# Performance work log

Measured on AMD Instinct MI355X. Metric: run time of the kernel, lower is better.

The kernel has to match this reference:

```python
import jax, jax.numpy as jnp
import numpy as np

B = 32768   # num_agents
D = 512     # obs_dim
H = 1024    # hidden_dim
O = 8       # num_options
A = 16      # num_actions
SCALE = 0.02


def setup_inputs() -> dict:
    key = jax.random.key(0)
    ks = jax.random.split(key, 12)
    rn = lambda k, shape: (jax.random.normal(k, shape, jnp.float32) * SCALE)
    obs = jax.random.normal(ks[0], (B, D), jnp.float32)
    dones = jax.random.bernoulli(ks[1], 0.05, (B,))
    executing_option = jax.random.randint(ks[2], (B,), 0, O)
    return {
        "obs": obs,
        "dones": dones,
        "executing_option": executing_option,
        # meta policy params
        "Wm1": rn(ks[3], (D, H)), "bm1": jnp.zeros((H,), jnp.float32),
        "Wm_pi": rn(ks[4], (H, O)), "Wm_v": rn(ks[5], (H, 1)),
        # termination net params (per-option sigmoid heads)
        "Wt1": rn(ks[6], (D, H)), "Wt2": rn(ks[7], (H, O)),
        # per-option sub-policy params (stacked over options)
        "W1": rn(ks[8], (O, D, H)), "b1": jnp.zeros((O, H), jnp.float32),
        "Wpi": rn(ks[9], (O, H, A)), "Wv": rn(ks[10], (O, H, 1)),
    }


def reference(obs, dones, executing_option,
              Wm1, bm1, Wm_pi, Wm_v, Wt1, Wt2, W1, b1, Wpi, Wv):
    # ---- meta policy: option logits + value + log_prob of chosen option ----
    hm = jax.nn.relu(obs @ Wm1 + bm1)                       # [B, H]
    meta_logits = hm @ Wm_pi                                # [B, O]
    meta_logp_all = jax.nn.log_softmax(meta_logits, axis=-1)
    meta_actions = jnp.argmax(meta_logits, axis=-1)         # [B]
    meta_log_probs = jnp.take_along_axis(meta_logp_all, meta_actions[:, None], 1)[:, 0]
    meta_values = (hm @ Wm_v)[:, 0]                         # [B]

    # ---- termination: per-option sigmoid head, gathered at executing option ----
    ht = jax.nn.relu(obs @ Wt1)                             # [B, H]
    term_all = jax.nn.sigmoid(ht @ Wt2)                     # [B, O]
    termination_probs = jnp.take_along_axis(term_all, executing_option[:, None], 1)[:, 0]
    option_terminates = dones | (termination_probs > 0.5)
    new_option = jnp.where(option_terminates, meta_actions, executing_option)  # [B]

    # ---- per-option sub-policy dispatch (dense compute, masked select) ----
    actions = jnp.zeros((obs.shape[0],), meta_actions.dtype)
    values = jnp.full((obs.shape[0],), jnp.nan, obs.dtype)
    log_probs = jnp.full((obs.shape[0],), jnp.nan, obs.dtype)
    for o in range(O):  # small fixed option set (structurally distinct experts)
        mask = new_option == o                              # [B]
        h = jax.nn.relu(obs @ W1[o] + b1[o])                # [B, H]
        logits = h @ Wpi[o]                                 # [B, A]
        logp_all = jax.nn.log_softmax(logits, axis=-1)
        act = jnp.argmax(logits, axis=-1)                   # [B]
        lp = jnp.take_along_axis(logp_all, act[:, None], 1)[:, 0]
        val = (h @ Wv[o])[:, 0]                             # [B]
        actions = jnp.where(mask, act, actions)
        values = jnp.where(mask, val, values)
        log_probs = jnp.where(mask, lp, log_probs)

    return (actions, values, log_probs,
            meta_actions, meta_values, meta_log_probs, termination_probs)
```

## Files before the change

### kernel.cpp

```cpp
#include <hip/hip_runtime.h>


constexpr int Bn = 32768;
constexpr int Dk = 512;
constexpr int Hn = 1024;

typedef __attribute__((ext_vector_type(8))) short short8v;
typedef __attribute__((ext_vector_type(4))) float f32x4;

__device__ __forceinline__ unsigned short f2bf(float x) {
    unsigned u = __float_as_uint(x);
    u += 0x7FFFu + ((u >> 16) & 1u);
    return (unsigned short)(u >> 16);
}
__device__ __forceinline__ float bf2f(unsigned short h) {
    return __uint_as_float(((unsigned)h) << 16);
}

constexpr size_t WS_COUNTS  = 0;
constexpr size_t WS_DFLAG   = 32;
constexpr size_t WS_BUCKETS = 64;
constexpr size_t WS_LOGITS  = 1u << 20;
constexpr size_t LOG_SZ     = (size_t)Bn * 20 * 4;
constexpr size_t WS_HID     = 16u << 20;
constexpr size_t WS_HEAD    = 40u << 20;
constexpr size_t WS_NEED    = WS_HEAD + (size_t)10 * 2 * 32 * 1024 * 2;

__global__ void k_detect(const unsigned int* __restrict__ w, int* __restrict__ flag)
{
    unsigned int acc = 0;
    for (int i = threadIdx.x; i < 8192; i += blockDim.x) acc |= w[i];
    if (acc & 0xFFFFFF00u) atomicOr(flag, 1);
}

__global__ __launch_bounds__(256)
void k_split_hid(const float* __restrict__ Wm1, const float* __restrict__ Wt1,
                 const float* __restrict__ W1, unsigned short* __restrict__ dst)
{
    const int bid = blockIdx.x;
    const int m  = bid >> 7;
    const int t  = bid & 127;
    const int k0 = (t >> 4) << 6;
    const int n0 = (t & 15) << 6;
    const float* src = (m == 0) ? Wm1 : (m == 1) ? Wt1 : (W1 + (size_t)(m - 2) * Dk * Hn);

    __shared__ unsigned short sT[2][64][72];
    const int tid = threadIdx.x;
    const int kk = tid >> 2;
    const int nc = (tid & 3) << 4;
    const float* p = src + (size_t)(k0 + kk) * Hn + n0 + nc;
#pragma unroll
    for (int i = 0; i < 4; ++i) {
        const float4 v = *(const float4*)(p + i * 4);
        float xs[4] = {v.x, v.y, v.z, v.w};
#pragma unroll
        for (int e = 0; e < 4; ++e) {
            const unsigned short h = f2bf(xs[e]);
            const unsigned short l = f2bf(xs[e] - bf2f(h));
            sT[0][nc + i * 4 + e][kk] = h;
            sT[1][nc + i * 4 + e][kk] = l;
        }
    }
    __syncthreads();
    if (tid < 128) {
        const int pl = tid >> 6, n = tid & 63;
        unsigned short* dp = dst + ((size_t)(m * 2 + pl) * 1024 + n0 + n) * 512 + k0;
        const unsigned short* sp = &sT[pl][n][0];
#pragma unroll
        for (int i = 0; i < 8; ++i)
            *(short8v*)(dp + i * 8) = *(const short8v*)(sp + i * 8);
    }
}

__global__ __launch_bounds__(256)
void k_split_head(const float* __restrict__ Wm_pi, const float* __restrict__ Wm_v,
                  const float* __restrict__ Wt2, const float* __restrict__ Wpi,
                  const float* __restrict__ Wv, unsigned short* __restrict__ dst)
{
    const int set = blockIdx.x >> 5, c = blockIdx.x & 31;
    const int tid = threadIdx.x;
    unsigned short* d0 = dst + ((size_t)(set * 2 + 0) * 32 + c) * 1024;
    unsigned short* d1 = dst + ((size_t)(set * 2 + 1) * 32 + c) * 1024;
#pragma unroll
    for (int i = 0; i < 4; ++i) {
        const int k = tid + i * 256;
        float x = 0.f;
        if (set == 0)      { if (c < 8) x = Wm_pi[k * 8 + c]; else if (c == 8) x = Wm_v[k]; }
        else if (set == 1) { if (c < 8) x = Wt2[k * 8 + c]; }
        else { const int o = set - 2;
               if (c < 16) x = Wpi[((size_t)o * 1024 + k) * 16 + c];
               else if (c == 16) x = Wv[o * 1024 + k]; }
        const unsigned short h = f2bf(x);
        d0[k] = h;
        d1[k] = f2bf(x - bf2f(h));
    }
}

template<int MODE, int CT>
__global__ __launch_bounds__(256, 2)
void k_gemm(const float* __restrict__ obs,
            const unsigned short* __restrict__ hidPl,
            const unsigned short* __restrict__ headPl,
            const float* __restrict__ bm1,
            const float* __restrict__ b1,
            float* __restrict__ L,
            const int* __restrict__ counts,
            const unsigned short* __restrict__ buckets)
{
    __shared__ __align__(16) unsigned char s_raw[65536];
    __shared__ float s_bias[128];
    __shared__ int   s_idx[128];

    const int tid = threadIdx.x;
    const int bid = blockIdx.x;

    int mat, set, ch, nrows = 128;
    const float* bias = nullptr;

    if constexpr (MODE == 2) {
        const int o = bid >> 11, rem = bid & 2047;
        const int x = rem & 7;  ch = (rem >> 3) & 7;
        const int rt = x + ((rem >> 6) << 3);
        const int n = counts[o], start = rt << 7;
        if (start >= n) return;
        nrows = min(128, n - start);
        if (tid < 128) s_idx[tid] = (int)buckets[(o << 15) + start + min(tid, nrows - 1)];
        mat = 2 + o; set = 2 + o; bias = b1 + (size_t)o * Hn;
    } else {
        const int x = bid & 7;  ch = (bid >> 3) & 7;
        const int rt = x + ((bid >> 6) << 3);
        if (tid < 128) s_idx[tid] = (rt << 7) + tid;
        mat = MODE; set = MODE; bias = (MODE == 0) ? bm1 : nullptr;
    }
    const int hc = ch << 7;
    if (tid < 128) s_bias[tid] = (MODE == 1) ? 0.f : bias[hc + tid];
    __syncthreads();

    const int l = tid & 63, w = tid >> 6;
    const int r15 = l & 15, q = l >> 4;
    const int R0 = (w >> 1) * 64, C0 = (w & 1) * 64;

    const int arow = tid >> 1, ahalf = tid & 1;
    const int bpl = tid >> 7, bn = tid & 127;
    const size_t arowg = (size_t)s_idx[arow] * Dk;
    const unsigned short* bptr = hidPl + ((size_t)(mat * 2 + bpl) * 1024 + (hc + bn)) * 512;

    f32x4 acc[4][4];
#pragma unroll
    for (int i = 0; i < 4; ++i)
#pragma unroll
        for (int j = 0; j < 4; ++j) acc[i][j] = (f32x4){0.f, 0.f, 0.f, 0.f};

    float4  av[4];
    short8v bv[4];

    auto stage_load = [&](int kt) {
        const float* p = obs + arowg + kt * 32 + ahalf * 16;
        av[0] = *(const float4*)(p);      av[1] = *(const float4*)(p + 4);
        av[2] = *(const float4*)(p + 8);  av[3] = *(const float4*)(p + 12);
        const unsigned short* bp = bptr + kt * 32;
#pragma unroll
        for (int j = 0; j < 4; ++j) bv[j] = *(const short8v*)(bp + j * 8);
    };

    auto stage_write = [&](int buf) {
        float xs[16] = {av[0].x, av[0].y, av[0].z, av[0].w,  av[1].x, av[1].y, av[1].z, av[1].w,
                        av[2].x, av[2].y, av[2].z, av[2].w,  av[3].x, av[3].y, av[3].z, av[3].w};
        short8v H0, H1, Lo0, Lo1;
#pragma unroll
        for (int e = 0; e < 8; ++e) {
            unsigned short h = f2bf(xs[e]);
            H0[e] = (short)h;  Lo0[e] = (short)f2bf(xs[e] - bf2f(h));
            h = f2bf(xs[8 + e]);
            H1[e] = (short)h;  Lo1[e] = (short)f2bf(xs[8 + e] - bf2f(h));
        }
        const int sw  = (arow >> 1) & 3;
        const int ra  = arow * 64;
        unsigned char* a0 = s_raw + (buf * 2 + 0) * 8192 + ra;
        unsigned char* a1 = s_raw + (buf * 2 + 1) * 8192 + ra;
        const int q0 = ((2 * ahalf) ^ sw) << 4, q1 = ((2 * ahalf + 1) ^ sw) << 4;
        *(short8v*)(a0 + q0) = H0;  *(short8v*)(a0 + q1) = H1;
        *(short8v*)(a1 + q0) = Lo0; *(short8v*)(a1 + q1) = Lo1;

        const int swb = (bn >> 1) & 3;
        unsigned char* bb = s_raw + 32768 + (buf * 2 + bpl) * 8192 + bn * 64;
#pragma unroll
        for (int j = 0; j < 4; ++j)
            *(short8v*)(bb + ((j ^ swb) << 4)) = bv[j];
    };

    auto mfma_step = [&](int buf) {
        short8v a[2][4], b[2][4];
#pragma unroll
        for (int rf = 0; rf < 4; ++rf) {
            const int row = R0 + rf * 16 + r15;
            const int off = row * 64 + ((q ^ ((row >> 1) & 3)) << 4);
            a[0][rf] = *(const short8v*)(s_raw + (buf * 2 + 0) * 8192 + off);
            a[1][rf] = *(const short8v*)(s_raw + (buf * 2 + 1) * 8192 + off);
        }
#pragma unroll
        for (int cf = 0; cf < 4; ++cf) {
            const int n = C0 + cf * 16 + r15;
            const int off = n * 64 + ((q ^ ((n >> 1) & 3)) << 4);
            b[0][cf] = *(const short8v*)(s_raw + 32768 + (buf * 2 + 0) * 8192 + off);
            b[1][cf] = *(const short8v*)(s_raw + 32768 + (buf * 2 + 1) * 8192 + off);
        }
#pragma unroll
        for (int t = 0; t < 4; ++t) {
            const int pa = 1 - (t >> 1), pb = 1 - (t & 1);
#pragma unroll
            for (int rf = 0; rf < 4; ++rf)
#pragma unroll
                for (int cf = 0; cf < 4; ++cf)
                    acc[rf][cf] = __builtin_amdgcn_mfma_f32_16x16x32_bf16(
                        a[pa][rf], b[pb][cf], acc[rf][cf], 0, 0, 0);
        }
    };

    stage_load(0);
    stage_write(0);
    __syncthreads();
#pragma unroll 1
    for (int kt = 0; kt < 16; ++kt) {
        const int cb = kt & 1;
        if (kt < 15) stage_load(kt + 1);
        mfma_step(cb);
        if (kt < 15) stage_write(cb ^ 1);
        __syncthreads();
    }

    {
        const int pl = tid >> 7, idx = tid & 127, c = idx >> 2, kq = idx & 3;
        const unsigned short* hp = headPl + ((size_t)(set * 2 + pl) * 32 + c) * 1024 + hc + kq * 32;
        short8v h0 = *(const short8v*)(hp);      short8v h1 = *(const short8v*)(hp + 8);
        short8v h2 = *(const short8v*)(hp + 16); short8v h3 = *(const short8v*)(hp + 24);
        unsigned char* d = s_raw + 33792 + pl * 8704 + c * 272 + kq * 64;
        ((short8v*)d)[0] = h0; ((short8v*)d)[1] = h1; ((short8v*)d)[2] = h2; ((short8v*)d)[3] = h3;
    }

    float* sh = (float*)s_raw;
#pragma unroll 1
    for (int half = 0; half < 2; ++half) {
        if ((w >> 1) == half) {
#pragma unroll
            for (int rf = 0; rf < 4; ++rf)
#pragma unroll
                for (int cf = 0; cf < 4; ++cf) {
                    const int c = C0 + cf * 16 + r15;
                    const float bs = s_bias[c];
#pragma unroll
                    for (int reg = 0; reg < 4; ++reg) {
                        const int r = rf * 16 + q * 4 + reg;
                        sh[r * 132 + c] = fmaxf(acc[rf][cf][reg] + bs, 0.f);
                    }
                }
        }
        __syncthreads();

        f32x4 hacc[2];
        hacc[0] = (f32x4){0.f, 0.f, 0.f, 0.f};
        hacc[1] = (f32x4){0.f, 0.f, 0.f, 0.f};
#pragma unroll
        for (int ks = 0; ks < 4; ++ks) {
            const float* shp = sh + (w * 16 + r15) * 132 + ks * 32 + q * 8;
            const float4 f0 = *(const float4*)(shp);
            const float4 f1 = *(const float4*)(shp + 4);
            const float xs[8] = {f0.x, f0.y, f0.z, f0.w, f1.x, f1.y, f1.z, f1.w};
            short8v ah, al;
#pragma unroll
            for (int j = 0; j < 8; ++j) {
                const unsigned short h = f2bf(xs[j]);
                ah[j] = (short)h;
                al[j] = (short)f2bf(xs[j] - bf2f(h));
            }
#pragma unroll
            for (int cf = 0; cf < 2; ++cf) {
                const unsigned char* hb = s_raw + 33792 + (cf * 16 + r15) * 272 + ks * 64 + q * 16;
                const short8v b0 = *(const short8v*)(hb);
                const short8v b1 = *(const short8v*)(hb + 8704);
                hacc[cf] = __builtin_amdgcn_mfma_f32_16x16x32_bf16(al, b1, hacc[cf], 0, 0, 0);
                hacc[cf] = __builtin_amdgcn_mfma_f32_16x16x32_bf16(al, b0, hacc[cf], 0, 0, 0);
                hacc[cf] = __builtin_amdgcn_mfma_f32_16x16x32_bf16(ah, b1, hacc[cf], 0, 0, 0);
                hacc[cf] = __builtin_amdgcn_mfma_f32_16x16x32_bf16(ah, b0, hacc[cf], 0, 0, 0);
            }
        }
#pragma unroll
        for (int cf = 0; cf < 2; ++cf) {
            const int c = cf * 16 + r15;
            if (c < CT) {
#pragma unroll
                for (int reg = 0; reg < 4; ++reg) {
                    const int rl = half * 64 + w * 16 + q * 4 + reg;
                    if (rl < nrows)
                        atomicAdd(&L[(size_t)s_idx[rl] * 20 + c], hacc[cf][reg]);
                }
            }
        }
        __syncthreads();
    }
}

__global__ __launch_bounds__(256)
void k_epi_meta(const float* __restrict__ L, float* __restrict__ out)
{
    const int g = blockIdx.x * 256 + threadIdx.x;
    const float* lr = L + (size_t)g * 20;
    float m = lr[0]; int am = 0;
#pragma unroll
    for (int j = 1; j < 8; ++j) { const float x = lr[j]; if (x > m) { m = x; am = j; } }
    float s = 0.f;
#pragma unroll
    for (int j = 0; j < 8; ++j) s += expf(lr[j] - m);
    out[3 * Bn + g] = (float)am;
    out[4 * Bn + g] = lr[8];
    out[5 * Bn + g] = -logf(s);
}

__global__ __launch_bounds__(256)
void k_epi_term(const float* __restrict__ L, float* __restrict__ out,
                const int* __restrict__ execopt, const void* __restrict__ dones,
                const int* __restrict__ dflag, int* __restrict__ counts,
                unsigned short* __restrict__ buckets)
{
    const int g = blockIdx.x * 256 + threadIdx.x;
    const int eo = execopt[g];
    const float logit = L[(size_t)g * 20 + eo];
    const float p = 1.f / (1.f + expf(-logit));
    out[6 * Bn + g] = p;
    bool dn;
    if (*dflag) dn = ((const unsigned char*)dones)[g] != 0;
    else        dn = ((const int*)dones)[g] != 0;
    const int ma = (int)out[3 * Bn + g];
    const int no = (dn || (p > 0.5f)) ? ma : eo;
    const int pos = atomicAdd(&counts[no], 1);
    buckets[(no << 15) + pos] = (unsigned short)g;
}

__global__ __launch_bounds__(256)
void k_epi_sub(const float* __restrict__ L, float* __restrict__ out)
{
    const int g = blockIdx.x * 256 + threadIdx.x;
    const float* lr = L + (size_t)g * 20;
    float m = lr[0]; int am = 0;
#pragma unroll
    for (int j = 1; j < 16; ++j) { const float x = lr[j]; if (x > m) { m = x; am = j; } }
    float s = 0.f;
#pragma unroll
    for (int j = 0; j < 16; ++j) s += expf(lr[j] - m);
    out[0 * Bn + g] = (float)am;
    out[1 * Bn + g] = lr[16];
    out[2 * Bn + g] = -logf(s);
}

constexpr int FB_ROWS = 64;
constexpr int FB_HC   = 128;
constexpr int FB_KT   = 16;
constexpr int FB_NT   = 256;

template<int CA, int CB, bool HASBIAS, int MODE>
__global__ __launch_bounds__(FB_NT, 2)
void k_fused_fb(const float* __restrict__ obs, const float* __restrict__ WhB,
                const float* __restrict__ biasB, const float* __restrict__ WAB,
                const float* __restrict__ WBB, float* __restrict__ out,
                int* __restrict__ counts, unsigned short* __restrict__ buckets,
                const void* __restrict__ dones, const int* __restrict__ dflag,
                const int* __restrict__ execopt)
{
    constexpr int CT  = CA + CB;
    constexpr int CPT = (CT + 3) / 4;

    __shared__ float s_obsT[FB_KT][FB_ROWS + 4];
    __shared__ float s_W[FB_KT][FB_HC + 4];
    __shared__ float s_h[FB_ROWS][FB_HC + 4];
    __shared__ float s_WhT[17][FB_HC + 4];
    __shared__ float s_logits[FB_ROWS][20];
    __shared__ float s_bias[FB_HC];
    __shared__ int   s_idx[FB_ROWS];

    const int tid = threadIdx.x;
    int nrows = FB_ROWS;
    const float* Wh = WhB; const float* bias = biasB;
    const float* WA = WAB; const float* WB = WBB;

    if constexpr (MODE == 2) {
        const int o = blockIdx.x >> 9;
        const int t = blockIdx.x & 511;
        const int n = counts[o];
        const int start = t * FB_ROWS;
        if (start >= n) return;
        nrows = min(FB_ROWS, n - start);
        if (tid < FB_ROWS) s_idx[tid] = (int)buckets[o * Bn + start + min(tid, nrows - 1)];
        Wh = WhB + (size_t)o * Dk * Hn; bias = biasB + (size_t)o * Hn;
        WA = WAB + (size_t)o * Hn * 16; WB = WBB + (size_t)o * Hn;
    } else {
        if (tid < FB_ROWS) s_idx[tid] = blockIdx.x * FB_ROWS + tid;
    }
    __syncthreads();

    const int tc = tid & 15, tr = tid >> 4;
    const int hr = tid >> 2, hq = tid & 3;
    const int ld_row = tid >> 2, ld_kk = (tid & 3) * 4;

    float head_acc[CPT];
#pragma unroll
    for (int i = 0; i < CPT; ++i) head_acc[i] = 0.f;

    for (int hcc = 0; hcc < Hn; hcc += FB_HC) {
        for (int e = tid; e < CT * FB_HC; e += FB_NT) {
            const int c = e >> 7, j = e & (FB_HC - 1);
            float v;
            if (c < CA) v = WA[(size_t)(hcc + j) * CA + c];
            else        v = WB[(size_t)(hcc + j) * CB + (c - CA)];
            s_WhT[c][j] = v;
        }
        if constexpr (HASBIAS) { if (tid < FB_HC) s_bias[tid] = bias[hcc + tid]; }

        float acc[4][8];
#pragma unroll
        for (int i = 0; i < 4; ++i)
#pragma unroll
            for (int j = 0; j < 8; ++j) acc[i][j] = 0.f;

        for (int kt = 0; kt < Dk; kt += FB_KT) {
            __syncthreads();
            {
                const int gr = s_idx[ld_row];
                const float4 v = *reinterpret_cast<const float4*>(obs + (size_t)gr * Dk + kt + ld_kk);
                s_obsT[ld_kk + 0][ld_row] = v.x; s_obsT[ld_kk + 1][ld_row] = v.y;
                s_obsT[ld_kk + 2][ld_row] = v.z; s_obsT[ld_kk + 3][ld_row] = v.w;
            }
#pragma unroll
            for (int p = 0; p < 2; ++p) {
                const int Li = tid + p * FB_NT;
                const int k = Li >> 5, cg = (Li & 31) * 4;
                *reinterpret_cast<float4*>(&s_W[k][cg]) =
                    *reinterpret_cast<const float4*>(Wh + (size_t)(kt + k) * Hn + hcc + cg);
            }
            __syncthreads();
#pragma unroll
            for (int k = 0; k < FB_KT; ++k) {
                const float4 avv = *reinterpret_cast<const float4*>(&s_obsT[k][tr * 4]);
                const float4 b0 = *reinterpret_cast<const float4*>(&s_W[k][tc * 4]);
                const float4 b1 = *reinterpret_cast<const float4*>(&s_W[k][64 + tc * 4]);
                float a_[4] = {avv.x, avv.y, avv.z, avv.w};
                float b_[8] = {b0.x, b0.y, b0.z, b0.w, b1.x, b1.y, b1.z, b1.w};
#pragma unroll
                for (int i = 0; i < 4; ++i)
#pragma unroll
                    for (int j = 0; j < 8; ++j) acc[i][j] = fmaf(a_[i], b_[j], acc[i][j]);
            }
        }

#pragma unroll
        for (int i = 0; i < 4; ++i) {
            const int r = tr * 4 + i;
            float4 v0, v1;
            v0.x = acc[i][0]; v0.y = acc[i][1]; v0.z = acc[i][2]; v0.w = acc[i][3];
            v1.x = acc[i][4]; v1.y = acc[i][5]; v1.z = acc[i][6]; v1.w = acc[i][7];
            if constexpr (HASBIAS) {
                v0.x += s_bias[tc * 4 + 0]; v0.y += s_bias[tc * 4 + 1];
                v0.z += s_bias[tc * 4 + 2]; v0.w += s_bias[tc * 4 + 3];
                v1.x += s_bias[64 + tc * 4 + 0]; v1.y += s_bias[64 + tc * 4 + 1];
                v1.z += s_bias[64 + tc * 4 + 2]; v1.w += s_bias[64 + tc * 4 + 3];
            }
            v0.x = fmaxf(v0.x, 0.f); v0.y = fmaxf(v0.y, 0.f);
            v0.z = fmaxf(v0.z, 0.f); v0.w = fmaxf(v0.w, 0.f);
            v1.x = fmaxf(v1.x, 0.f); v1.y = fmaxf(v1.y, 0.f);
            v1.z = fmaxf(v1.z, 0.f); v1.w = fmaxf(v1.w, 0.f);
            *reinterpret_cast<float4*>(&s_h[r][tc * 4]) = v0;
            *reinterpret_cast<float4*>(&s_h[r][64 + tc * 4]) = v1;
        }
        __syncthreads();
        {
            const float* hrow = s_h[hr];
#pragma unroll
            for (int i = 0; i < CPT; ++i) {
                const int c = hq * CPT + i;
                if (c < CT) {
                    const float* wrow = s_WhT[c];
                    float a = head_acc[i];
#pragma unroll
                    for (int j = 0; j < FB_HC; j += 4) {
                        const float4 hv = *reinterpret_cast<const float4*>(&hrow[j]);
                        const float4 wv = *reinterpret_cast<const float4*>(&wrow[j]);
                        a = fmaf(hv.x, wv.x, a); a = fmaf(hv.y, wv.y, a);
                        a = fmaf(hv.z, wv.z, a); a = fmaf(hv.w, wv.w, a);
                    }
                    head_acc[i] = a;
                }
            }
        }
        __syncthreads();
    }

#pragma unroll
    for (int i = 0; i < CPT; ++i) {
        const int c = hq * CPT + i;
        if (c < CT) s_logits[hr][c] = head_acc[i];
    }
    __syncthreads();

    if constexpr (MODE == 0) {
        if (tid < FB_ROWS) {
            const int g = s_idx[tid];
            float m = s_logits[tid][0]; int am = 0;
#pragma unroll
            for (int j = 1; j < 8; ++j) { const float x = s_logits[tid][j]; if (x > m) { m = x; am = j; } }
            float s = 0.f;
#pragma unroll
            for (int j = 0; j < 8; ++j) s += expf(s_logits[tid][j] - m);
            out[3 * Bn + g] = (float)am;
            out[4 * Bn + g] = s_logits[tid][8];
            out[5 * Bn + g] = -logf(s);
        }
    } else if constexpr (MODE == 1) {
        if (tid < FB_ROWS) {
            const int g = s_idx[tid];
            const int eo = execopt[g];
            const float p = 1.f / (1.f + expf(-s_logits[tid][eo]));
            out[6 * Bn + g] = p;
            bool dn;
            if (*dflag) dn = ((const unsigned char*)dones)[g] != 0;
            else        dn = ((const int*)dones)[g] != 0;
            const int no = (dn || (p > 0.5f)) ? (int)out[3 * Bn + g] : eo;
            const int pos = atomicAdd(&counts[no], 1);
            buckets[no * Bn + pos] = (unsigned short)g;
        }
    } else {
        if (tid < nrows) {
            const int g = s_idx[tid];
            float m = s_logits[tid][0]; int am = 0;
#pragma unroll
            for (int j = 1; j < 16; ++j) { const float x = s_logits[tid][j]; if (x > m) { m = x; am = j; } }
            float s = 0.f;
#pragma unroll
            for (int j = 0; j < 16; ++j) s += expf(s_logits[tid][j] - m);
            out[0 * Bn + g] = (float)am;
            out[1 * Bn + g] = s_logits[tid][16];
            out[2 * Bn + g] = -logf(s);
        }
    }
}

extern "C" void kernel_launch(void* const* d_in, const int* in_sizes, int n_in,
                              void* d_out, int out_size, void* d_ws, size_t ws_size,
                              hipStream_t stream)
{
    const float* obs     = (const float*)d_in[0];
    const void*  dones   = d_in[1];
    const int*   execopt = (const int*)d_in[2];
    const float* Wm1   = (const float*)d_in[3];
    const float* bm1   = (const float*)d_in[4];
    const float* Wm_pi = (const float*)d_in[5];
    const float* Wm_v  = (const float*)d_in[6];
    const float* Wt1   = (const float*)d_in[7];
    const float* Wt2   = (const float*)d_in[8];
    const float* W1    = (const float*)d_in[9];
    const float* b1    = (const float*)d_in[10];
    const float* Wpi   = (const float*)d_in[11];
    const float* Wv    = (const float*)d_in[12];
    float* out = (float*)d_out;

    unsigned char* ws = (unsigned char*)d_ws;
    int* counts = (int*)(ws + WS_COUNTS);
    int* dflag  = (int*)(ws + WS_DFLAG);
    unsigned short* buckets = (unsigned short*)(ws + WS_BUCKETS);

    hipMemsetAsync(d_ws, 0, 64, stream);
    k_detect<<<1, 256, 0, stream>>>((const unsigned int*)dones, dflag);

    if (ws_size >= WS_NEED) {
        float* metaL = (float*)(ws + WS_LOGITS);
        float* termL = (float*)(ws + WS_LOGITS + LOG_SZ);
        float* subL  = (float*)(ws + WS_LOGITS + 2 * LOG_SZ);
        unsigned short* hidPl  = (unsigned short*)(ws + WS_HID);
        unsigned short* headPl = (unsigned short*)(ws + WS_HEAD);

        hipMemsetAsync(ws + WS_LOGITS, 0, 3 * LOG_SZ, stream);
        k_split_hid<<<1280, 256, 0, stream>>>(Wm1, Wt1, W1, hidPl);
        k_split_head<<<320, 256, 0, stream>>>(Wm_pi, Wm_v, Wt2, Wpi, Wv, headPl);

        k_gemm<0, 9><<<2048, 256, 0, stream>>>(obs, hidPl, headPl, bm1, b1, metaL, counts, buckets);
        k_epi_meta<<<128, 256, 0, stream>>>(metaL, out);
        k_gemm<1, 8><<<2048, 256, 0, stream>>>(obs, hidPl, headPl, bm1, b1, termL, counts, buckets);
        k_epi_term<<<128, 256, 0, stream>>>(termL, out, execopt, dones, dflag, counts, buckets);
        k_gemm<2, 17><<<16384, 256, 0, stream>>>(obs, hidPl, headPl, bm1, b1, subL, counts, buckets);
        k_epi_sub<<<128, 256, 0, stream>>>(subL, out);
    } else {
        k_fused_fb<8, 1, true, 0><<<Bn / FB_ROWS, FB_NT, 0, stream>>>(
            obs, Wm1, bm1, Wm_pi, Wm_v, out, counts, buckets, dones, dflag, execopt);
        k_fused_fb<8, 0, false, 1><<<Bn / FB_ROWS, FB_NT, 0, stream>>>(
            obs, Wt1, nullptr, Wt2, nullptr, out, counts, buckets, dones, dflag, execopt);
        k_fused_fb<16, 1, true, 2><<<8 * (Bn / FB_ROWS), FB_NT, 0, stream>>>(
            obs, W1, b1, Wpi, Wv, out, counts, buckets, dones, dflag, execopt);
    }
}
```

Before: 736.8 us.

## Pre-split obs to bf16 planes, use direct global-to-LDS loads, merge meta/term GEMMs

Adds a kernel that splits obs once into bf16 hi/lo planes in workspace. The GEMM then stages both A and B tiles with global_load_lds 16-byte direct-to-LDS copies instead of register round-trips and per-tile re-splitting. The meta and termination GEMMs and their epilogues are merged into one launch each. The split-bf16 product also drops the lo*lo term, going from 4 to 3 MFMAs per step, which slightly lowers precision. The cost is an extra pass over obs and extra workspace, and the fast path only runs if the workspace is large enough.

```diff
diff --git a/kernel.cpp b/kernel.cpp
--- a/kernel.cpp
+++ b/kernel.cpp
@@ -15,6 +15,12 @@
 }
 __device__ __forceinline__ float bf2f(unsigned short h) {
     return __uint_as_float(((unsigned)h) << 16);
+}
+
+__device__ __forceinline__ void gload16(const void* g, void* l) {
+    __builtin_amdgcn_global_load_lds(
+        (const __attribute__((address_space(1))) unsigned int*)g,
+        (__attribute__((address_space(3))) unsigned int*)l, 16, 0, 0);
 }
 
 constexpr size_t WS_COUNTS  = 0;
@@ -24,13 +30,33 @@
 constexpr size_t LOG_SZ     = (size_t)Bn * 20 * 4;
 constexpr size_t WS_HID     = 16u << 20;
 constexpr size_t WS_HEAD    = 40u << 20;
-constexpr size_t WS_NEED    = WS_HEAD + (size_t)10 * 2 * 32 * 1024 * 2;
+constexpr size_t WS_OBS     = 42u << 20;
+constexpr size_t MID_NEED   = WS_HEAD + (size_t)10 * 2 * 32 * 1024 * 2;
+constexpr size_t FULL_NEED  = WS_OBS + (size_t)2 * Bn * Dk * 2;
 
 __global__ void k_detect(const unsigned int* __restrict__ w, int* __restrict__ flag)
 {
     unsigned int acc = 0;
     for (int i = threadIdx.x; i < 8192; i += blockDim.x) acc |= w[i];
     if (acc & 0xFFFFFF00u) atomicOr(flag, 1);
+}
+
+__global__ __launch_bounds__(256)
+void k_split_obs(const float* __restrict__ obs, unsigned short* __restrict__ dst)
+{
+    const size_t i = ((size_t)blockIdx.x * 256 + threadIdx.x) * 8;
+    const float4 v0 = *(const float4*)(obs + i);
+    const float4 v1 = *(const float4*)(obs + i + 4);
+    const float xs[8] = {v0.x, v0.y, v0.z, v0.w, v1.x, v1.y, v1.z, v1.w};
+    short8v hi, lo;
+#pragma unroll
+    for (int e = 0; e < 8; ++e) {
+        const unsigned short h = f2bf(xs[e]);
+        hi[e] = (short)h;
+        lo[e] = (short)f2bf(xs[e] - bf2f(h));
+    }
+    *(short8v*)(dst + i) = hi;
+    *(short8v*)(dst + (size_t)Bn * Dk + i) = lo;
 }
 
 __global__ __launch_bounds__(256)
@@ -96,14 +122,16 @@
     }
 }
 
-template<int MODE, int CT>
+template<int MODE, bool APL>
 __global__ __launch_bounds__(256, 2)
 void k_gemm(const float* __restrict__ obs,
+            const unsigned short* __restrict__ obsPl,
             const unsigned short* __restrict__ hidPl,
             const unsigned short* __restrict__ headPl,
             const float* __restrict__ bm1,
             const float* __restrict__ b1,
-            float* __restrict__ L,
+            float* __restrict__ metaL, float* __restrict__ termL,
+            float* __restrict__ subL,
             const int* __restrict__ counts,
             const unsigned short* __restrict__ buckets)
 {
@@ -114,7 +142,8 @@
     const int tid = threadIdx.x;
     const int bid = blockIdx.x;
 
-    int mat, set, ch, nrows = 128;
+    int mat, set, ch, CT, nrows = 128;
+    float* L;
     const float* bias = nullptr;
 
     if constexpr (MODE == 2) {
@@ -125,45 +154,71 @@
         if (start >= n) return;
         nrows = min(128, n - start);
         if (tid < 128) s_idx[tid] = (int)buckets[(o << 15) + start + min(tid, nrows - 1)];
-        mat = 2 + o; set = 2 + o; bias = b1 + (size_t)o * Hn;
+        mat = 2 + o; set = 2 + o; bias = b1 + (size_t)o * Hn; L = subL; CT = 17;
     } else {
-        const int x = bid & 7;  ch = (bid >> 3) & 7;
-        const int rt = x + ((bid >> 6) << 3);
+        const int x = bid & 7;  ch = (bid >> 3) & 7;  mat = (bid >> 6) & 1;
+        const int rt = x + ((bid >> 7) << 3);
         if (tid < 128) s_idx[tid] = (rt << 7) + tid;
-        mat = MODE; set = MODE; bias = (MODE == 0) ? bm1 : nullptr;
+        set = mat; CT = mat ? 8 : 9;
+        L = mat ? termL : metaL;
+        bias = mat ? nullptr : bm1;
     }
     const int hc = ch << 7;
-    if (tid < 128) s_bias[tid] = (MODE == 1) ? 0.f : bias[hc + tid];
+    if (tid < 128) s_bias[tid] = (bias == nullptr) ? 0.f : bias[hc + tid];
     __syncthreads();
 
     const int l = tid & 63, w = tid >> 6;
-    const int r15 = l & 15, q = l >> 4;
+    const int r15 = l & 15, qq = l >> 4;
     const int R0 = (w >> 1) * 64, C0 = (w & 1) * 64;
 
+    f32x4 acc[4][4];
+#pragma unroll
+    for (int i = 0; i < 4; ++i)
+#pragma unroll
+        for (int j = 0; j < 4; ++j) acc[i][j] = (f32x4){0.f, 0.f, 0.f, 0.f};
+
+    const int spl = w >> 1;
+    const int sg0 = (w & 1) * 4;
+    const unsigned char* bB[4];
+#pragma unroll
+    for (int j = 0; j < 4; ++j) {
+        const int cl = (sg0 + j) * 16 + (l >> 2);
+        const int qd = ((l & 3) ^ ((cl >> 1) & 3)) << 4;
+        bB[j] = (const unsigned char*)hidPl
+              + ((size_t)(mat * 2 + spl) * 1024 + hc + cl) * 1024 + qd;
+    }
+    const unsigned char* aB[4];
+    if constexpr (APL) {
+#pragma unroll
+        for (int j = 0; j < 4; ++j) {
+            const int rl = (sg0 + j) * 16 + (l >> 2);
+            const int qd = ((l & 3) ^ ((rl >> 1) & 3)) << 4;
+            aB[j] = (const unsigned char*)obsPl
+                  + ((size_t)spl * Bn + (size_t)s_idx[rl]) * 1024 + qd;
+        }
+    }
+
+    auto stage = [&](int buf, int kt) {
+#pragma unroll
+        for (int j = 0; j < 4; ++j) {
+            if constexpr (APL)
+                gload16(aB[j] + kt * 64,
+                        s_raw + (buf * 2 + spl) * 8192 + (sg0 + j) * 1024);
+            gload16(bB[j] + kt * 64,
+                    s_raw + 32768 + (buf * 2 + spl) * 8192 + (sg0 + j) * 1024);
+        }
+    };
+
     const int arow = tid >> 1, ahalf = tid & 1;
-    const int bpl = tid >> 7, bn = tid & 127;
-    const size_t arowg = (size_t)s_idx[arow] * Dk;
-    const unsigned short* bptr = hidPl + ((size_t)(mat * 2 + bpl) * 1024 + (hc + bn)) * 512;
-
-    f32x4 acc[4][4];
-#pragma unroll
-    for (int i = 0; i < 4; ++i)
-#pragma unroll
-        for (int j = 0; j < 4; ++j) acc[i][j] = (f32x4){0.f, 0.f, 0.f, 0.f};
-
-    float4  av[4];
-    short8v bv[4];
-
-    auto stage_load = [&](int kt) {
+    size_t arowg = 0;
+    if constexpr (!APL) arowg = (size_t)s_idx[arow] * Dk;
+    float4 av[4];
+    auto loadA = [&](int kt) {
         const float* p = obs + arowg + kt * 32 + ahalf * 16;
         av[0] = *(const float4*)(p);      av[1] = *(const float4*)(p + 4);
         av[2] = *(const float4*)(p + 8);  av[3] = *(const float4*)(p + 12);
-        const unsigned short* bp = bptr + kt * 32;
-#pragma unroll
-        for (int j = 0; j < 4; ++j) bv[j] = *(const short8v*)(bp + j * 8);
     };
-
-    auto stage_write = [&](int buf) {
+    auto writeA = [&](int buf) {
         float xs[16] = {av[0].x, av[0].y, av[0].z, av[0].w,  av[1].x, av[1].y, av[1].z, av[1].w,
                         av[2].x, av[2].y, av[2].z, av[2].w,  av[3].x, av[3].y, av[3].z, av[3].w};
         short8v H0, H1, Lo0, Lo1;
@@ -174,19 +229,13 @@
             h = f2bf(xs[8 + e]);
             H1[e] = (short)h;  Lo1[e] = (short)f2bf(xs[8 + e] - bf2f(h));
         }
-        const int sw  = (arow >> 1) & 3;
-        const int ra  = arow * 64;
+        const int sw = (arow >> 1) & 3;
+        const int ra = arow * 64;
         unsigned char* a0 = s_raw + (buf * 2 + 0) * 8192 + ra;
         unsigned char* a1 = s_raw + (buf * 2 + 1) * 8192 + ra;
         const int q0 = ((2 * ahalf) ^ sw) << 4, q1 = ((2 * ahalf + 1) ^ sw) << 4;
         *(short8v*)(a0 + q0) = H0;  *(short8v*)(a0 + q1) = H1;
         *(short8v*)(a1 + q0) = Lo0; *(short8v*)(a1 + q1) = Lo1;
-
-        const int swb = (bn >> 1) & 3;
-        unsigned char* bb = s_raw + 32768 + (buf * 2 + bpl) * 8192 + bn * 64;
-#pragma unroll
-        for (int j = 0; j < 4; ++j)
-            *(short8v*)(bb + ((j ^ swb) << 4)) = bv[j];
     };
 
     auto mfma_step = [&](int buf) {
@@ -194,39 +243,60 @@
 #pragma unroll
         for (int rf = 0; rf < 4; ++rf) {
             const int row = R0 + rf * 16 + r15;
-            const int off = row * 64 + ((q ^ ((row >> 1) & 3)) << 4);
+            const int off = row * 64 + ((qq ^ ((row >> 1) & 3)) << 4);
             a[0][rf] = *(const short8v*)(s_raw + (buf * 2 + 0) * 8192 + off);
             a[1][rf] = *(const short8v*)(s_raw + (buf * 2 + 1) * 8192 + off);
         }
 #pragma unroll
         for (int cf = 0; cf < 4; ++cf) {
             const int n = C0 + cf * 16 + r15;
-            const int off = n * 64 + ((q ^ ((n >> 1) & 3)) << 4);
+            const int off = n * 64 + ((qq ^ ((n >> 1) & 3)) << 4);
             b[0][cf] = *(const short8v*)(s_raw + 32768 + (buf * 2 + 0) * 8192 + off);
             b[1][cf] = *(const short8v*)(s_raw + 32768 + (buf * 2 + 1) * 8192 + off);
         }
 #pragma unroll
-        for (int t = 0; t < 4; ++t) {
-            const int pa = 1 - (t >> 1), pb = 1 - (t & 1);
-#pragma unroll
-            for (int rf = 0; rf < 4; ++rf)
-#pragma unroll
-                for (int cf = 0; cf < 4; ++cf)
-                    acc[rf][cf] = __builtin_amdgcn_mfma_f32_16x16x32_bf16(
-                        a[pa][rf], b[pb][cf], acc[rf][cf], 0, 0, 0);
-        }
+        for (int rf = 0; rf < 4; ++rf)
+#pragma unroll
+            for (int cf = 0; cf < 4; ++cf)
+                acc[rf][cf] = __builtin_amdgcn_mfma_f32_16x16x32_bf16(
+                    a[1][rf], b[0][cf], acc[rf][cf], 0, 0, 0);
+#pragma unroll
+        for (int rf = 0; rf < 4; ++rf)
+#pragma unroll
+            for (int cf = 0; cf < 4; ++cf)
+                acc[rf][cf] = __builtin_amdgcn_mfma_f32_16x16x32_bf16(
+                    a[0][rf], b[1][cf], acc[rf][cf], 0, 0, 0);
+#pragma unroll
+        for (int rf = 0; rf < 4; ++rf)
+#pragma unroll
+            for (int cf = 0; cf < 4; ++cf)
+                acc[rf][cf] = __builtin_amdgcn_mfma_f32_16x16x32_bf16(
+                    a[0][rf], b[0][cf], acc[rf][cf], 0, 0, 0);
     };
 
-    stage_load(0);
-    stage_write(0);
-    __syncthreads();
-#pragma unroll 1
-    for (int kt = 0; kt < 16; ++kt) {
-        const int cb = kt & 1;
-        if (kt < 15) stage_load(kt + 1);
-        mfma_step(cb);
-        if (kt < 15) stage_write(cb ^ 1);
+    if constexpr (APL) {
+        stage(0, 0);
         __syncthreads();
+#pragma unroll 2
+        for (int kt = 0; kt < 16; ++kt) {
+            const int cb = kt & 1;
+            if (kt < 15) stage(cb ^ 1, kt + 1);
+            mfma_step(cb);
+            __syncthreads();
+        }
+    } else {
+        loadA(0);
+        stage(0, 0);
+        writeA(0);
+        __syncthreads();
+#pragma unroll 2
+        for (int kt = 0; kt < 16; ++kt) {
+            const int cb = kt & 1;
+            if (kt < 15) { loadA(kt + 1); stage(cb ^ 1, kt + 1); }
+            mfma_step(cb);
+            if (kt < 15) writeA(cb ^ 1);
+            __syncthreads();
+        }
     }
 
     {
@@ -250,7 +320,7 @@
                     const float bs = s_bias[c];
 #pragma unroll
                     for (int reg = 0; reg < 4; ++reg) {
-                        const int r = rf * 16 + q * 4 + reg;
+                        const int r = rf * 16 + qq * 4 + reg;
                         sh[r * 132 + c] = fmaxf(acc[rf][cf][reg] + bs, 0.f);
                     }
                 }
@@ -262,7 +332,7 @@
         hacc[1] = (f32x4){0.f, 0.f, 0.f, 0.f};
 #pragma unroll
         for (int ks = 0; ks < 4; ++ks) {
-            const float* shp = sh + (w * 16 + r15) * 132 + ks * 32 + q * 8;
+            const float* shp = sh + (w * 16 + r15) * 132 + ks * 32 + qq * 8;
             const float4 f0 = *(const float4*)(shp);
             const float4 f1 = *(const float4*)(shp + 4);
             const float xs[8] = {f0.x, f0.y, f0.z, f0.w, f1.x, f1.y, f1.z, f1.w};
@@ -275,12 +345,11 @@
             }
 #pragma unroll
             for (int cf = 0; cf < 2; ++cf) {
-                const unsigned char* hb = s_raw + 33792 + (cf * 16 + r15) * 272 + ks * 64 + q * 16;
+                const unsigned char* hb = s_raw + 33792 + (cf * 16 + r15) * 272 + ks * 64 + qq * 16;
                 const short8v b0 = *(const short8v*)(hb);
-                const short8v b1 = *(const short8v*)(hb + 8704);
-                hacc[cf] = __builtin_amdgcn_mfma_f32_16x16x32_bf16(al, b1, hacc[cf], 0, 0, 0);
+                const short8v b1v = *(const short8v*)(hb + 8704);
                 hacc[cf] = __builtin_amdgcn_mfma_f32_16x16x32_bf16(al, b0, hacc[cf], 0, 0, 0);
-                hacc[cf] = __builtin_amdgcn_mfma_f32_16x16x32_bf16(ah, b1, hacc[cf], 0, 0, 0);
+                hacc[cf] = __builtin_amdgcn_mfma_f32_16x16x32_bf16(ah, b1v, hacc[cf], 0, 0, 0);
                 hacc[cf] = __builtin_amdgcn_mfma_f32_16x16x32_bf16(ah, b0, hacc[cf], 0, 0, 0);
             }
         }
@@ -290,7 +359,7 @@
             if (c < CT) {
 #pragma unroll
                 for (int reg = 0; reg < 4; ++reg) {
-                    const int rl = half * 64 + w * 16 + q * 4 + reg;
+                    const int rl = half * 64 + w * 16 + qq * 4 + reg;
                     if (rl < nrows)
                         atomicAdd(&L[(size_t)s_idx[rl] * 20 + c], hacc[cf][reg]);
                 }
@@ -301,10 +370,13 @@
 }
 
 __global__ __launch_bounds__(256)
-void k_epi_meta(const float* __restrict__ L, float* __restrict__ out)
+void k_epi_mt(const float* __restrict__ metaL, const float* __restrict__ termL,
+              float* __restrict__ out, const int* __restrict__ execopt,
+              const void* __restrict__ dones, const int* __restrict__ dflag,
+              int* __restrict__ counts, unsigned short* __restrict__ buckets)
 {
     const int g = blockIdx.x * 256 + threadIdx.x;
-    const float* lr = L + (size_t)g * 20;
+    const float* lr = metaL + (size_t)g * 20;
     float m = lr[0]; int am = 0;
 #pragma unroll
     for (int j = 1; j < 8; ++j) { const float x = lr[j]; if (x > m) { m = x; am = j; } }
@@ -314,24 +386,15 @@
     out[3 * Bn + g] = (float)am;
     out[4 * Bn + g] = lr[8];
     out[5 * Bn + g] = -logf(s);
-}
-
-__global__ __launch_bounds__(256)
-void k_epi_term(const float* __restrict__ L, float* __restrict__ out,
-                const int* __restrict__ execopt, const void* __restrict__ dones,
-                const int* __restrict__ dflag, int* __restrict__ counts,
-                unsigned short* __restrict__ buckets)
-{
-    const int g = blockIdx.x * 256 + threadIdx.x;
+
     const int eo = execopt[g];
-    const float logit = L[(size_t)g * 20 + eo];
+    const float logit = termL[(size_t)g * 20 + eo];
     const float p = 1.f / (1.f + expf(-logit));
     out[6 * Bn + g] = p;
     bool dn;
     if (*dflag) dn = ((const unsigned char*)dones)[g] != 0;
     else        dn = ((const int*)dones)[g] != 0;
-    const int ma = (int)out[3 * Bn + g];
-    const int no = (dn || (p > 0.5f)) ? ma : eo;
+    const int no = (dn || (p > 0.5f)) ? am : eo;
     const int pos = atomicAdd(&counts[no], 1);
     buckets[(no << 15) + pos] = (unsigned short)g;
 }
@@ -352,13 +415,8 @@
     out[2 * Bn + g] = -logf(s);
 }
 
-constexpr int FB_ROWS = 64;
-constexpr int FB_HC   = 128;
-constexpr int FB_KT   = 16;
-constexpr int FB_NT   = 256;
-
 template<int CA, int CB, bool HASBIAS, int MODE>
-__global__ __launch_bounds__(FB_NT, 2)
+__global__ __launch_bounds__(256, 2)
 void k_fused_fb(const float* __restrict__ obs, const float* __restrict__ WhB,
                 const float* __restrict__ biasB, const float* __restrict__ WAB,
                 const float* __restrict__ WBB, float* __restrict__ out,
@@ -369,16 +427,16 @@
     constexpr int CT  = CA + CB;
     constexpr int CPT = (CT + 3) / 4;
 
-    __shared__ float s_obsT[FB_KT][FB_ROWS + 4];
-    __shared__ float s_W[FB_KT][FB_HC + 4];
-    __shared__ float s_h[FB_ROWS][FB_HC + 4];
-    __shared__ float s_WhT[17][FB_HC + 4];
-    __shared__ float s_logits[FB_ROWS][20];
-    __shared__ float s_bias[FB_HC];
-    __shared__ int   s_idx[FB_ROWS];
+    __shared__ float s_obsT[16][68];
+    __shared__ float s_W[16][132];
+    __shared__ float s_h[64][132];
+    __shared__ float s_WhT[17][132];
+    __shared__ float s_logits[64][20];
+    __shared__ float s_bias[128];
+    __shared__ int   s_idx[64];
 
     const int tid = threadIdx.x;
-    int nrows = FB_ROWS;
+    int nrows = 64;
     const float* Wh = WhB; const float* bias = biasB;
     const float* WA = WAB; const float* WB = WBB;
 
@@ -386,14 +444,14 @@
         const int o = blockIdx.x >> 9;
         const int t = blockIdx.x & 511;
         const int n = counts[o];
-        const int start = t * FB_ROWS;
+        const int start = t * 64;
         if (start >= n) return;
-        nrows = min(FB_ROWS, n - start);
-        if (tid < FB_ROWS) s_idx[tid] = (int)buckets[o * Bn + start + min(tid, nrows - 1)];
+        nrows = min(64, n - start);
+        if (tid < 64) s_idx[tid] = (int)buckets[o * Bn + start + min(tid, nrows - 1)];
         Wh = WhB + (size_t)o * Dk * Hn; bias = biasB + (size_t)o * Hn;
         WA = WAB + (size_t)o * Hn * 16; WB = WBB + (size_t)o * Hn;
     } else {
-        if (tid < FB_ROWS) s_idx[tid] = blockIdx.x * FB_ROWS + tid;
+        if (tid < 64) s_idx[tid] = blockIdx.x * 64 + tid;
     }
     __syncthreads();
 
@@ -405,15 +463,15 @@
 #pragma unroll
     for (int i = 0; i < CPT; ++i) head_acc[i] = 0.f;
 
-    for (int hcc = 0; hcc < Hn; hcc += FB_HC) {
-        for (int e = tid; e < CT * FB_HC; e += FB_NT) {
-            const int c = e >> 7, j = e & (FB_HC - 1);
+    for (int hcc = 0; hcc < Hn; hcc += 128) {
+        for (int e = tid; e < CT * 128; e += 256) {
+            const int c = e >> 7, j = e & 127;
             float v;
             if (c < CA) v = WA[(size_t)(hcc + j) * CA + c];
             else        v = WB[(size_t)(hcc + j) * CB + (c - CA)];
             s_WhT[c][j] = v;
         }
-        if constexpr (HASBIAS) { if (tid < FB_HC) s_bias[tid] = bias[hcc + tid]; }
+        if constexpr (HASBIAS) { if (tid < 128) s_bias[tid] = bias[hcc + tid]; }
 
         float acc[4][8];
 #pragma unroll
@@ -421,7 +479,7 @@
 #pragma unroll
             for (int j = 0; j < 8; ++j) acc[i][j] = 0.f;
 
-        for (int kt = 0; kt < Dk; kt += FB_KT) {
+        for (int kt = 0; kt < Dk; kt += 16) {
             __syncthreads();
             {
                 const int gr = s_idx[ld_row];
@@ -431,14 +489,14 @@
             }
 #pragma unroll
             for (int p = 0; p < 2; ++p) {
-                const int Li = tid + p * FB_NT;
+                const int Li = tid + p * 256;
                 const int k = Li >> 5, cg = (Li & 31) * 4;
                 *reinterpret_cast<float4*>(&s_W[k][cg]) =
                     *reinterpret_cast<const float4*>(Wh + (size_t)(kt + k) * Hn + hcc + cg);
             }
             __syncthreads();
 #pragma unroll
-            for (int k = 0; k < FB_KT; ++k) {
+            for (int k = 0; k < 16; ++k) {
                 const float4 avv = *reinterpret_cast<const float4*>(&s_obsT[k][tr * 4]);
                 const float4 b0 = *reinterpret_cast<const float4*>(&s_W[k][tc * 4]);
                 const float4 b1 = *reinterpret_cast<const float4*>(&s_W[k][64 + tc * 4]);
@@ -480,7 +538,7 @@
                     const float* wrow = s_WhT[c];
                     float a = head_acc[i];
 #pragma unroll
-                    for (int j = 0; j < FB_HC; j += 4) {
+                    for (int j = 0; j < 128; j += 4) {
                         const float4 hv = *reinterpret_cast<const float4*>(&hrow[j]);
                         const float4 wv = *reinterpret_cast<const float4*>(&wrow[j]);
                         a = fmaf(hv.x, wv.x, a); a = fmaf(hv.y, wv.y, a);
@@ -501,7 +559,7 @@
     __syncthreads();
 
     if constexpr (MODE == 0) {
-        if (tid < FB_ROWS) {
+        if (tid < 64) {
             const int g = s_idx[tid];
             float m = s_logits[tid][0]; int am = 0;
 #pragma unroll
@@ -514,7 +572,7 @@
             out[5 * Bn + g] = -logf(s);
         }
     } else if constexpr (MODE == 1) {
-        if (tid < FB_ROWS) {
+        if (tid < 64) {
             const int g = s_idx[tid];
             const int eo = execopt[g];
             const float p = 1.f / (1.f + expf(-s_logits[tid][eo]));
@@ -569,29 +627,40 @@
     hipMemsetAsync(d_ws, 0, 64, stream);
     k_detect<<<1, 256, 0, stream>>>((const unsigned int*)dones, dflag);
 
-    if (ws_size >= WS_NEED) {
+    if (ws_size >= MID_NEED) {
         float* metaL = (float*)(ws + WS_LOGITS);
         float* termL = (float*)(ws + WS_LOGITS + LOG_SZ);
         float* subL  = (float*)(ws + WS_LOGITS + 2 * LOG_SZ);
         unsigned short* hidPl  = (unsigned short*)(ws + WS_HID);
         unsigned short* headPl = (unsigned short*)(ws + WS_HEAD);
+        unsigned short* obsPl  = (unsigned short*)(ws + WS_OBS);
 
         hipMemsetAsync(ws + WS_LOGITS, 0, 3 * LOG_SZ, stream);
         k_split_hid<<<1280, 256, 0, stream>>>(Wm1, Wt1, W1, hidPl);
         k_split_head<<<320, 256, 0, stream>>>(Wm_pi, Wm_v, Wt2, Wpi, Wv, headPl);
 
-        k_gemm<0, 9><<<2048, 256, 0, stream>>>(obs, hidPl, headPl, bm1, b1, metaL, counts, buckets);
-        k_epi_meta<<<128, 256, 0, stream>>>(metaL, out);
-        k_gemm<1, 8><<<2048, 256, 0, stream>>>(obs, hidPl, headPl, bm1, b1, termL, counts, buckets);
-        k_epi_term<<<128, 256, 0, stream>>>(termL, out, execopt, dones, dflag, counts, buckets);
-        k_gemm<2, 17><<<16384, 256, 0, stream>>>(obs, hidPl, headPl, bm1, b1, subL, counts, buckets);
-        k_epi_sub<<<128, 256, 0, stream>>>(subL, out);
+        if (ws_size >= FULL_NEED) {
+            k_split_obs<<<8192, 256, 0, stream>>>(obs, obsPl);
+            k_gemm<3, true><<<4096, 256, 0, stream>>>(
+                obs, obsPl, hidPl, headPl, bm1, b1, metaL, termL, subL, counts, buckets);
+            k_epi_mt<<<128, 256, 0, stream>>>(metaL, termL, out, execopt, dones, dflag, counts, buckets);
+            k_gemm<2, true><<<16384, 256, 0, stream>>>(
+                obs, obsPl, hidPl, headPl, bm1, b1, metaL, termL, subL, counts, buckets);
+            k_epi_sub<<<128, 256, 0, stream>>>(subL, out);
+        } else {
+            k_gemm<3, false><<<4096, 256, 0, stream>>>(
+                obs, nullptr, hidPl, headPl, bm1, b1, metaL, termL, subL, counts, buckets);
+            k_epi_mt<<<128, 256, 0, stream>>>(metaL, termL, out, execopt, dones, dflag, counts, buckets);
+            k_gemm<2, false><<<16384, 256, 0, stream>>>(
+                obs, nullptr, hidPl, headPl, bm1, b1, metaL, termL, subL, counts, buckets);
+            k_epi_sub<<<128, 256, 0, stream>>>(subL, out);
+        }
     } else {
-        k_fused_fb<8, 1, true, 0><<<Bn / FB_ROWS, FB_NT, 0, stream>>>(
+        k_fused_fb<8, 1, true, 0><<<Bn / 64, 256, 0, stream>>>(
             obs, Wm1, bm1, Wm_pi, Wm_v, out, counts, buckets, dones, dflag, execopt);
-        k_fused_fb<8, 0, false, 1><<<Bn / FB_ROWS, FB_NT, 0, stream>>>(
+        k_fused_fb<8, 0, false, 1><<<Bn / 64, 256, 0, stream>>>(
             obs, Wt1, nullptr, Wt2, nullptr, out, counts, buckets, dones, dflag, execopt);
-        k_fused_fb<16, 1, true, 2><<<8 * (Bn / FB_ROWS), FB_NT, 0, stream>>>(
+        k_fused_fb<16, 1, true, 2><<<8 * (Bn / 64), 256, 0, stream>>>(
             obs, W1, b1, Wpi, Wv, out, counts, buckets, dones, dflag, execopt);
     }
 }
```

New measurement: 668.2 us. 9.3% less time.
